# Kernel optimization log

Hardware: AMD Instinct MI355X
Metric: run time of the kernel (lower is better)

Reference implementation:

```python
import jax, jax.numpy as jnp
import numpy as np

DIM = 256
KEY_DIM = 16
NUM_HEADS = 8
ATTN_RATIO = 4
NH_KD = KEY_DIM * NUM_HEADS   # 128
D = ATTN_RATIO * KEY_DIM      # 64
DH = D * NUM_HEADS            # 512
POS_LEN = 16
SCALE = KEY_DIM ** -0.5


def _cbn(x, w, s, b):
    # 1x1 conv (no bias) + folded BatchNorm affine. w: [out,in], x: [B,in,H,W]
    y = jnp.einsum('oi,bihw->bohw', w, x)
    return y * s[None, :, None, None] + b[None, :, None, None]


def _interp_pos(pos, n):
    # F.interpolate(mode='linear', align_corners=False) from length POS_LEN to n.
    L = pos.shape[-1]
    coords = (jnp.arange(n, dtype=pos.dtype) + 0.5) * (L / n) - 0.5
    coords = jnp.clip(coords, 0.0, L - 1)
    lo = jnp.floor(coords).astype(jnp.int32)
    hi = jnp.minimum(lo + 1, L - 1)
    t = coords - lo.astype(pos.dtype)
    return pos[..., lo] * (1 - t) + pos[..., hi] * t  # [1,C,n]


def _axial_attn(q_emb, k_emb, v_emb, pos_q, pos_k, n):
    # q_emb/k_emb: [B,NH_KD,n], v_emb: [B,DH,n]
    B = q_emb.shape[0]
    q = (q_emb + _interp_pos(pos_q, n)).reshape(B, NUM_HEADS, KEY_DIM, n)
    k = (k_emb + _interp_pos(pos_k, n)).reshape(B, NUM_HEADS, KEY_DIM, n)
    v = v_emb.reshape(B, NUM_HEADS, D, n)
    attn = jnp.einsum('bhcn,bhcm->bhnm', q, k) * SCALE
    attn = jax.nn.softmax(attn, axis=-1)
    xx = jnp.einsum('bhnm,bhdm->bhnd', attn, v)      # [B,NH,n,D]
    return xx.transpose(0, 1, 3, 2).reshape(B, DH, n)  # [B,DH,n]


def _forward(x, wq, sq, bq, wk, sk, bk, wv, sv, bv,
             pos_rowq, pos_rowk, pos_colq, pos_colk,
             w_row, s_row, b_row, w_col, s_col, b_col,
             w_proj, s_proj, b_proj, w_sc, s_sc, b_sc,
             w_dw, s_dw, b_dw, w_pw, s_pw, b_pw):
    B, C, H, W = x.shape
    q = _cbn(x, wq, sq, bq)   # [B,NH_KD,H,W]
    k = _cbn(x, wk, sk, bk)
    v = _cbn(x, wv, sv, bv)   # [B,DH,H,W]

    # row branch (mean over W)
    xx_row = _axial_attn(q.mean(-1), k.mean(-1), v.mean(-1), pos_rowq, pos_rowk, H)
    xx_row = _cbn(jax.nn.relu(xx_row[..., None]), w_row, s_row, b_row)      # [B,DH,H,1]
    # column branch (mean over H)
    xx_col = _axial_attn(q.mean(-2), k.mean(-2), v.mean(-2), pos_colq, pos_colk, W)
    xx_col = _cbn(jax.nn.relu(xx_col[:, :, None, :]), w_col, s_col, b_col)  # [B,DH,1,W]

    attn_out = v + (xx_row + xx_col)
    attn_out = _cbn(jax.nn.relu(attn_out), w_proj, s_proj, b_proj)          # [B,DIM,H,W]

    # gate branch: 1x1 -> dw3x3 -> relu -> 1x1 -> h_sigmoid
    gate = _cbn(x, w_sc, s_sc, b_sc)
    gate = jax.lax.conv_general_dilated(
        gate, w_dw, (1, 1), 'SAME',
        dimension_numbers=('NCHW', 'OIHW', 'NCHW'), feature_group_count=DIM)
    gate = gate * s_dw[None, :, None, None] + b_dw[None, :, None, None]
    gate = jax.nn.relu(gate)
    gate = _cbn(gate, w_pw, s_pw, b_pw)
    gate = jnp.clip(gate + 3.0, 0.0, 6.0) / 6.0  # h_sigmoid
    return gate * attn_out


def setup_inputs() -> dict:
    key = jax.random.key(0)
    ks = jax.random.split(key, 32)
    B, H, W = 16, 64, 64
    nrm = lambda k, sh, sc=0.05: jax.random.normal(k, sh, dtype=jnp.float32) * sc
    inp = {
        'x': nrm(ks[0], (B, DIM, H, W), 1.0),
        'wq': nrm(ks[1], (NH_KD, DIM)), 'sq': 1.0 + nrm(ks[2], (NH_KD,)), 'bq': nrm(ks[3], (NH_KD,)),
        'wk': nrm(ks[4], (NH_KD, DIM)), 'sk': 1.0 + nrm(ks[5], (NH_KD,)), 'bk': nrm(ks[6], (NH_KD,)),
        'wv': nrm(ks[7], (DH, DIM)), 'sv': 1.0 + nrm(ks[8], (DH,)), 'bv': nrm(ks[9], (DH,)),
        'pos_rowq': nrm(ks[10], (1, NH_KD, POS_LEN), 1.0), 'pos_rowk': nrm(ks[11], (1, NH_KD, POS_LEN), 1.0),
        'pos_colq': nrm(ks[12], (1, NH_KD, POS_LEN), 1.0), 'pos_colk': nrm(ks[13], (1, NH_KD, POS_LEN), 1.0),
        'w_row': nrm(ks[14], (DH, DH)), 's_row': 1.0 + nrm(ks[15], (DH,)), 'b_row': nrm(ks[16], (DH,)),
        'w_col': nrm(ks[17], (DH, DH)), 's_col': 1.0 + nrm(ks[18], (DH,)), 'b_col': nrm(ks[19], (DH,)),
        'w_proj': nrm(ks[20], (DIM, DH)), 's_proj': 1.0 + nrm(ks[21], (DIM,)), 'b_proj': nrm(ks[22], (DIM,)),
        'w_sc': nrm(ks[23], (DIM, DIM)), 's_sc': 1.0 + nrm(ks[24], (DIM,)), 'b_sc': nrm(ks[25], (DIM,)),
        'w_dw': nrm(ks[26], (DIM, 1, 3, 3)), 's_dw': 1.0 + nrm(ks[27], (DIM,)), 'b_dw': nrm(ks[28], (DIM,)),
        'w_pw': nrm(ks[29], (DIM, DIM)), 's_pw': 1.0 + nrm(ks[30], (DIM,)), 'b_pw': nrm(ks[31], (DIM,)),
    }
    return inp


def reference(x, wq, sq, bq, wk, sk, bk, wv, sv, bv,
              pos_rowq, pos_rowk, pos_colq, pos_colk,
              w_row, s_row, b_row, w_col, s_col, b_col,
              w_proj, s_proj, b_proj, w_sc, s_sc, b_sc,
              w_dw, s_dw, b_dw, w_pw, s_pw, b_pw):
    return _forward(x, wq, sq, bq, wk, sk, bk, wv, sv, bv,
                    pos_rowq, pos_rowk, pos_colq, pos_colk,
                    w_row, s_row, b_row, w_col, s_col, b_col,
                    w_proj, s_proj, b_proj, w_sc, s_sc, b_sc,
                    w_dw, s_dw, b_dw, w_pw, s_pw, b_pw)
```

## Files before the change

kernel.cpp:

```cpp
#include <hip/hip_runtime.h>
#include <math.h>

typedef unsigned short u16;
typedef unsigned int u32;
typedef short short8 __attribute__((ext_vector_type(8)));
typedef float f32x4 __attribute__((ext_vector_type(4)));

#define Bn 16
#define Cc 256
#define Pp 4096
#define DHc 512
#define PTOT 65536
#define SCALE 0.25f

__device__ __forceinline__ float bf2f(u16 u) {
    return __uint_as_float(((u32)u) << 16);
}
__device__ __forceinline__ u16 f2bf(float f) {
    u32 u = __float_as_uint(f);
    u32 lsb = (u >> 16) & 1u;
    u += 0x7fffu + lsb;
    return (u16)(u >> 16);
}

__device__ __forceinline__ void gload16(const u16* g, u16* l) {
    __builtin_amdgcn_global_load_lds(
        (const __attribute__((address_space(1))) void*)(uintptr_t)g,
        (__attribute__((address_space(3))) void*)(u32)(uintptr_t)l,
        16, 0, 0);
}

__global__ __launch_bounds__(256) void mean_kernel(
    const float* __restrict__ x, u16* __restrict__ xmb) {
    __shared__ float plane[64][65];
    int bc = blockIdx.x;
    int b = bc >> 8, c = bc & 255;
    const float* xp = x + (size_t)bc * Pp;
    int tid = threadIdx.x;
#pragma unroll
    for (int k = 0; k < 16; ++k) {
        int idx = tid + k * 256;
        plane[idx >> 6][idx & 63] = xp[idx];
    }
    __syncthreads();
    if (tid < 64) {
        float s = 0.f;
#pragma unroll
        for (int w = 0; w < 64; ++w) s += plane[tid][w];
        xmb[((size_t)b * 64 + tid) * 256 + c] = f2bf(s * (1.f / 64.f));
    } else if (tid < 128) {
        int w = tid - 64;
        float s = 0.f;
#pragma unroll
        for (int h = 0; h < 64; ++h) s += plane[h][w];
        xmb[((size_t)1024 + b * 64 + w) * 256 + c] = f2bf(s * (1.f / 64.f));
    }
}

__global__ __launch_bounds__(256) void xpose_kernel(
    const float* __restrict__ x, u16* __restrict__ xbf) {
    __shared__ float tile[64][65];
    int pb = blockIdx.x;
    int cb = blockIdx.y;
    int b = blockIdx.z;
    int t = threadIdx.x;
    int p_l = t & 63, c_q = t >> 6;
    const float* xp = x + ((size_t)b * Cc + cb * 64) * Pp + pb * 64;
#pragma unroll
    for (int rr = 0; rr < 16; ++rr) {
        int c_l = rr * 4 + c_q;
        tile[p_l][c_l] = xp[(size_t)c_l * Pp + p_l];
    }
    __syncthreads();
    int c_l2 = t & 63, p_q = t >> 6;
    u16* dst = xbf + ((size_t)b * Pp + pb * 64) * Cc + cb * 64;
#pragma unroll
    for (int rr = 0; rr < 16; ++rr) {
        int p_l2 = rr * 4 + p_q;
        dst[(size_t)p_l2 * Cc + c_l2] = f2bf(tile[p_l2][c_l2]);
    }
}

__global__ __launch_bounds__(256) void wconv_kernel(
    const float* __restrict__ wq, const float* __restrict__ wk, const float* __restrict__ wv,
    const float* __restrict__ wsc, const float* __restrict__ wproj, const float* __restrict__ wpw,
    const float* __restrict__ wrow, const float* __restrict__ wcol,
    const float* __restrict__ wdw,
    u16* __restrict__ wqkvb, u16* __restrict__ wscb,
    u16* __restrict__ wprojb, u16* __restrict__ wpwb,
    u16* __restrict__ wrb, u16* __restrict__ wcb, float* __restrict__ wdwT) {
    int t = blockIdx.x * 256 + threadIdx.x;
    if (t < 2304) wdwT[(t % 9) * 256 + (t / 9)] = wdw[t];
    if (t < 32768) wqkvb[t] = f2bf(wq[t]);
    else if (t < 65536) wqkvb[t] = f2bf(wk[t - 32768]);
    else if (t < 196608) wqkvb[t] = f2bf(wv[t - 65536]);
    else if (t < 262144) wscb[t - 196608] = f2bf(wsc[t - 196608]);
    else if (t < 393216) wprojb[t - 262144] = f2bf(wproj[t - 262144]);
    else if (t < 458752) wpwb[t - 393216] = f2bf(wpw[t - 393216]);
    else if (t < 720896) wrb[t - 458752] = f2bf(wrow[t - 458752]);
    else wcb[t - 720896] = f2bf(wcol[t - 720896]);
}

__device__ __forceinline__ void gemm_mainloop(
    const u16* __restrict__ W, const u16* __restrict__ X, int K,
    int o0, size_t prow0, u16* ldsA, u16* ldsB, f32x4 (&acc)[4][4]) {
    int t = threadIdx.x;
    int w = t >> 6, lane = t & 63;
    int sr = (w << 5) + (lane >> 2);
    int ks = (lane & 3) * 8;
    const u16* gA = W + (size_t)(o0 + sr) * K + ks;
    const u16* gB = X + (prow0 + sr) * K + ks;
    u16* lA = ldsA + sr * 32 + ks;
    u16* lB = ldsB + sr * 32 + ks;
    int wo = (w >> 1) * 64, wp = (w & 1) * 64;
    const u16* fA = ldsA + (wo + (lane & 15)) * 32 + ((lane >> 4) * 8);
    const u16* fB = ldsB + (wp + (lane & 15)) * 32 + ((lane >> 4) * 8);

    for (int k0 = 0; k0 < K; k0 += 32) {
        if (k0) __syncthreads();
        gload16(gA + k0, lA);
        gload16(gA + k0 + (size_t)16 * K, lA + 16 * 32);
        gload16(gB + k0, lB);
        gload16(gB + k0 + (size_t)16 * K, lB + 16 * 32);
        __syncthreads();
        short8 a[4], b[4];
#pragma unroll
        for (int i = 0; i < 4; ++i) a[i] = *(const short8*)(fA + i * 16 * 32);
#pragma unroll
        for (int j = 0; j < 4; ++j) b[j] = *(const short8*)(fB + j * 16 * 32);
#pragma unroll
        for (int i = 0; i < 4; ++i)
#pragma unroll
            for (int j = 0; j < 4; ++j)
                acc[i][j] = __builtin_amdgcn_mfma_f32_16x16x32_bf16(a[i], b[j], acc[i][j], 0, 0, 0);
    }
}

__global__ __launch_bounds__(256) void gemm_qkv(
    const u16* __restrict__ Wb, const u16* __restrict__ X,
    const float* __restrict__ sq, const float* __restrict__ bq,
    const float* __restrict__ sk, const float* __restrict__ bk,
    const float* __restrict__ sv, const float* __restrict__ bv,
    const float* __restrict__ posrq, const float* __restrict__ posrk,
    const float* __restrict__ poscq, const float* __restrict__ posck,
    float* __restrict__ qrow, float* __restrict__ krow, float* __restrict__ vrow,
    float* __restrict__ qcol, float* __restrict__ kcol, float* __restrict__ vcol) {
    __shared__ u16 ldsA[128 * 32];
    __shared__ u16 ldsB[128 * 32];
    f32x4 acc[4][4];
#pragma unroll
    for (int i = 0; i < 4; ++i)
#pragma unroll
        for (int j = 0; j < 4; ++j) acc[i][j] = (f32x4){0.f, 0.f, 0.f, 0.f};
    int o0 = blockIdx.x * 128;
    size_t prow0 = (size_t)blockIdx.y * 128;
    gemm_mainloop(Wb, X, 256, o0, prow0, ldsA, ldsB, acc);

    int lane = threadIdx.x & 63, w = threadIdx.x >> 6;
    int wo = (w >> 1) * 64, wp = (w & 1) * 64;
    int quad = lane >> 4, cn = lane & 15;
#pragma unroll
    for (int j = 0; j < 4; ++j) {
        int p = (int)prow0 + wp + j * 16 + cn;
        int branch = p >> 10, loc = p & 1023;
        int b = loc >> 6, n = loc & 63;
        float coords = 0.25f * (float)n - 0.375f;
        coords = fminf(fmaxf(coords, 0.f), 15.f);
        int lo = (int)floorf(coords);
        int hi = min(lo + 1, 15);
        float tt = coords - (float)lo;
#pragma unroll
        for (int i = 0; i < 4; ++i) {
            int o = o0 + wo + i * 16 + quad * 4;
            if (o < 128) {
                const float* pos = branch ? poscq : posrq;
                float* dst = branch ? qcol : qrow;
#pragma unroll
                for (int r = 0; r < 4; ++r) {
                    int c = o + r;
                    float pv = pos[c * 16 + lo] * (1.f - tt) + pos[c * 16 + hi] * tt;
                    dst[b * 8192 + c * 64 + n] = acc[i][j][r] * sq[c] + bq[c] + pv;
                }
            } else if (o < 256) {
                const float* pos = branch ? posck : posrk;
                float* dst = branch ? kcol : krow;
#pragma unroll
                for (int r = 0; r < 4; ++r) {
                    int c = o - 128 + r;
                    float pv = pos[c * 16 + lo] * (1.f - tt) + pos[c * 16 + hi] * tt;
                    dst[b * 8192 + c * 64 + n] = acc[i][j][r] * sk[c] + bk[c] + pv;
                }
            } else {
                float* dst = branch ? vcol : vrow;
#pragma unroll
                for (int r = 0; r < 4; ++r) {
                    int c = o - 256 + r;
                    dst[b * 32768 + c * 64 + n] = acc[i][j][r] * sv[c] + bv[c];
                }
            }
        }
    }
}

__global__ __launch_bounds__(512) void attn_kernel(
    const float* __restrict__ qr, const float* __restrict__ kr, const float* __restrict__ vr,
    const float* __restrict__ qc, const float* __restrict__ kc, const float* __restrict__ vc,
    u16* __restrict__ xxbf) {
    int branch = blockIdx.y;
    const float* q = branch ? qc : qr;
    const float* k = branch ? kc : kr;
    const float* v = branch ? vc : vr;
    int bh = blockIdx.x;
    int b = bh >> 3, h = bh & 7;
    __shared__ float qs[16][64], ks[16][64], vs[64][64];
    int t = threadIdx.x;
#pragma unroll
    for (int i = t; i < 1024; i += 512) {
        int c = i >> 6, nn = i & 63;
        qs[c][nn] = q[b * 8192 + (h * 16 + c) * 64 + nn];
        ks[c][nn] = k[b * 8192 + (h * 16 + c) * 64 + nn];
    }
#pragma unroll
    for (int i = t; i < 4096; i += 512) {
        int d = i >> 6, nn = i & 63;
        vs[d][nn] = v[b * 32768 + (h * 64 + d) * 64 + nn];
    }
    __syncthreads();

    int n = t & 63, dq = t >> 6;
    float qv[16];
#pragma unroll
    for (int c = 0; c < 16; ++c) qv[c] = qs[c][n];

    float s[64];
    float mx = -1e30f;
    for (int m = 0; m < 64; ++m) {
        float acc = 0.f;
#pragma unroll
        for (int c = 0; c < 16; ++c) acc += qv[c] * ks[c][m];
        acc *= SCALE;
        s[m] = acc;
        mx = fmaxf(mx, acc);
    }
    float sum = 0.f;
    for (int m = 0; m < 64; ++m) {
        s[m] = __expf(s[m] - mx);
        sum += s[m];
    }
    float inv = 1.f / sum;
    u16* dst = xxbf + (((size_t)(b * 2 + branch)) * 64 + n) * 512 + h * 64 + dq * 8;
#pragma unroll
    for (int dd = 0; dd < 8; ++dd) {
        int d = dq * 8 + dd;
        float acc = 0.f;
#pragma unroll 8
        for (int m = 0; m < 64; ++m) acc += s[m] * vs[d][m];
        dst[dd] = f2bf(fmaxf(acc * inv, 0.f));
    }
}

__global__ __launch_bounds__(256) void post_gemm(
    const u16* __restrict__ xxbf, const u16* __restrict__ wrb, const u16* __restrict__ wcb,
    const float* __restrict__ s_row, const float* __restrict__ b_row,
    const float* __restrict__ s_col, const float* __restrict__ b_col,
    float* __restrict__ xr2, float* __restrict__ xc2) {
    __shared__ u16 ldsA[64 * 32];
    __shared__ u16 ldsB[256 * 32];
    int o0 = blockIdx.x * 256;
    int b = blockIdx.y;
    int branch = blockIdx.z;
    const u16* A = xxbf + ((size_t)(b * 2 + branch)) * 64 * 512;
    const u16* W = branch ? wcb : wrb;
    const float* ss = branch ? s_col : s_row;
    const float* bb = branch ? b_col : b_row;
    float* dst = (branch ? xc2 : xr2) + (size_t)b * 32768;

    f32x4 acc[4][4];
#pragma unroll
    for (int i = 0; i < 4; ++i)
#pragma unroll
        for (int j = 0; j < 4; ++j) acc[i][j] = (f32x4){0.f, 0.f, 0.f, 0.f};

    int t = threadIdx.x, w = t >> 6, lane = t & 63;
    int ks = (t & 3) * 8;
    const u16* gA = A + (size_t)(t >> 2) * 512 + ks;
    const u16* gB = W + (size_t)(o0 + (t >> 2)) * 512 + ks;
    u16* lA = ldsA + (t >> 2) * 32 + ks;
    u16* lB = ldsB + (t >> 2) * 32 + ks;
    const u16* fA = ldsA + (lane & 15) * 32 + ((lane >> 4) * 8);
    const u16* fB = ldsB + (w * 64 + (lane & 15)) * 32 + ((lane >> 4) * 8);

    for (int k0 = 0; k0 < 512; k0 += 32) {
        if (k0) __syncthreads();
        gload16(gA + k0, lA);
#pragma unroll
        for (int r = 0; r < 4; ++r)
            gload16(gB + k0 + (size_t)r * 64 * 512, lB + r * 64 * 32);
        __syncthreads();
        short8 a[4], bfr[4];
#pragma unroll
        for (int i = 0; i < 4; ++i) a[i] = *(const short8*)(fA + i * 16 * 32);
#pragma unroll
        for (int j = 0; j < 4; ++j) bfr[j] = *(const short8*)(fB + j * 16 * 32);
#pragma unroll
        for (int i = 0; i < 4; ++i)
#pragma unroll
            for (int j = 0; j < 4; ++j)
                acc[i][j] = __builtin_amdgcn_mfma_f32_16x16x32_bf16(a[i], bfr[j], acc[i][j], 0, 0, 0);
    }

    int quad = lane >> 4, cn = lane & 15;
#pragma unroll
    for (int i = 0; i < 4; ++i)
#pragma unroll
        for (int j = 0; j < 4; ++j) {
            int o = o0 + w * 64 + j * 16 + cn;
            float sv_ = ss[o], bv_ = bb[o];
#pragma unroll
            for (int r = 0; r < 4; ++r) {
                int n = i * 16 + quad * 4 + r;
                dst[n * 512 + o] = acc[i][j][r] * sv_ + bv_;
            }
        }
}

__global__ __launch_bounds__(256) void gemm_sc(
    const u16* __restrict__ Wb, const u16* __restrict__ X,
    const float* __restrict__ s, const float* __restrict__ bb, u16* __restrict__ outb) {
    __shared__ u16 ldsA[128 * 32];
    __shared__ u16 ldsB[128 * 32];
    f32x4 acc[4][4];
#pragma unroll
    for (int i = 0; i < 4; ++i)
#pragma unroll
        for (int j = 0; j < 4; ++j) acc[i][j] = (f32x4){0.f, 0.f, 0.f, 0.f};
    int o0 = blockIdx.x * 128;
    size_t prow0 = (size_t)blockIdx.y * 128;
    gemm_mainloop(Wb, X, 256, o0, prow0, ldsA, ldsB, acc);

    int lane = threadIdx.x & 63, w = threadIdx.x >> 6;
    int wo = (w >> 1) * 64, wp = (w & 1) * 64;
    int quad = lane >> 4, cn = lane & 15;
#pragma unroll
    for (int i = 0; i < 4; ++i) {
        int ob = o0 + wo + i * 16 + quad * 4;
        f32x4 s4 = *(const f32x4*)&s[ob];
        f32x4 b4 = *(const f32x4*)&bb[ob];
#pragma unroll
        for (int j = 0; j < 4; ++j) {
            size_t p = prow0 + wp + j * 16 + cn;
            ushort4 o4;
            o4.x = f2bf(acc[i][j][0] * s4[0] + b4[0]);
            o4.y = f2bf(acc[i][j][1] * s4[1] + b4[1]);
            o4.z = f2bf(acc[i][j][2] * s4[2] + b4[2]);
            o4.w = f2bf(acc[i][j][3] * s4[3] + b4[3]);
            *(ushort4*)&outb[p * 256 + ob] = o4;
        }
    }
}

__global__ __launch_bounds__(256) void gemm_pw(
    const u16* __restrict__ Wb, const u16* __restrict__ X,
    const float* __restrict__ s, const float* __restrict__ bb, u16* __restrict__ outb) {
    __shared__ u16 ldsA[128 * 32];
    __shared__ u16 ldsB[128 * 32];
    f32x4 acc[4][4];
#pragma unroll
    for (int i = 0; i < 4; ++i)
#pragma unroll
        for (int j = 0; j < 4; ++j) acc[i][j] = (f32x4){0.f, 0.f, 0.f, 0.f};
    int o0 = blockIdx.x * 128;
    size_t prow0 = (size_t)blockIdx.y * 128;
    gemm_mainloop(Wb, X, 256, o0, prow0, ldsA, ldsB, acc);

    int lane = threadIdx.x & 63, w = threadIdx.x >> 6;
    int wo = (w >> 1) * 64, wp = (w & 1) * 64;
    int quad = lane >> 4, cn = lane & 15;
#pragma unroll
    for (int i = 0; i < 4; ++i) {
        int ob = o0 + wo + i * 16 + quad * 4;
        f32x4 s4 = *(const f32x4*)&s[ob];
        f32x4 b4 = *(const f32x4*)&bb[ob];
#pragma unroll
        for (int j = 0; j < 4; ++j) {
            size_t p = prow0 + wp + j * 16 + cn;
            ushort4 o4;
            o4.x = f2bf(fminf(fmaxf(acc[i][j][0] * s4[0] + b4[0] + 3.f, 0.f), 6.f) * (1.f / 6.f));
            o4.y = f2bf(fminf(fmaxf(acc[i][j][1] * s4[1] + b4[1] + 3.f, 0.f), 6.f) * (1.f / 6.f));
            o4.z = f2bf(fminf(fmaxf(acc[i][j][2] * s4[2] + b4[2] + 3.f, 0.f), 6.f) * (1.f / 6.f));
            o4.w = f2bf(fminf(fmaxf(acc[i][j][3] * s4[3] + b4[3] + 3.f, 0.f), 6.f) * (1.f / 6.f));
            *(ushort4*)&outb[p * 256 + ob] = o4;
        }
    }
}

__global__ __launch_bounds__(512) void fused_vproj(
    const u16* __restrict__ Wv, const u16* __restrict__ Wp,
    const u16* __restrict__ X,
    const float* __restrict__ sv, const float* __restrict__ bv,
    const float* __restrict__ xr2, const float* __restrict__ xc2,
    const float* __restrict__ sp, const float* __restrict__ bp,
    const u16* __restrict__ gate, float* __restrict__ out) {
    __shared__ u16 abt[64 * 512];
    __shared__ u16 ldsA[512 * 32];
    __shared__ u16 ldsB[64 * 32];

    int t = threadIdx.x;
    int lane = t & 63, w = t >> 6;
    int quad = lane >> 4, cn = lane & 15;
    int p0 = blockIdx.x * 64;
    int bi = p0 >> 12;
    int hh = (p0 >> 6) & 63;

    f32x4 acc1[4][4];
#pragma unroll
    for (int i = 0; i < 4; ++i)
#pragma unroll
        for (int j = 0; j < 4; ++j) acc1[i][j] = (f32x4){0.f, 0.f, 0.f, 0.f};

    int rowA = t >> 2, seg = t & 3;
    int ow = w * 64;
    const u16* fA = ldsA + (ow + cn) * 32 + quad * 8;
    const u16* fB = ldsB + cn * 32 + quad * 8;

    for (int k0 = 0; k0 < 256; k0 += 32) {
        if (k0) __syncthreads();
#pragma unroll
        for (int kk = 0; kk < 4; ++kk)
            gload16(Wv + (size_t)(rowA + kk * 128) * 256 + k0 + seg * 8,
                    ldsA + ((size_t)t + kk * 512) * 8);
        if (t < 256)
            gload16(X + ((size_t)p0 + rowA) * 256 + k0 + seg * 8, ldsB + (size_t)t * 8);
        __syncthreads();
        short8 a[4], b[4];
#pragma unroll
        for (int i = 0; i < 4; ++i) a[i] = *(const short8*)(fA + i * 16 * 32);
#pragma unroll
        for (int j = 0; j < 4; ++j) b[j] = *(const short8*)(fB + j * 16 * 32);
#pragma unroll
        for (int i = 0; i < 4; ++i)
#pragma unroll
            for (int j = 0; j < 4; ++j)
                acc1[i][j] = __builtin_amdgcn_mfma_f32_16x16x32_bf16(a[i], b[j], acc1[i][j], 0, 0, 0);
    }

#pragma unroll
    for (int i = 0; i < 4; ++i) {
        int ob = ow + i * 16 + quad * 4;
        f32x4 s4 = *(const f32x4*)&sv[ob];
        f32x4 b4 = *(const f32x4*)&bv[ob];
        f32x4 ra = *(const f32x4*)&xr2[(size_t)bi * 32768 + hh * 512 + ob];
#pragma unroll
        for (int j = 0; j < 4; ++j) {
            int p = j * 16 + cn;
            f32x4 ca = *(const f32x4*)&xc2[(size_t)bi * 32768 + p * 512 + ob];
            ushort4 o4;
            o4.x = f2bf(fmaxf(acc1[i][j][0] * s4[0] + b4[0] + ra[0] + ca[0], 0.f));
            o4.y = f2bf(fmaxf(acc1[i][j][1] * s4[1] + b4[1] + ra[1] + ca[1], 0.f));
            o4.z = f2bf(fmaxf(acc1[i][j][2] * s4[2] + b4[2] + ra[2] + ca[2], 0.f));
            o4.w = f2bf(fmaxf(acc1[i][j][3] * s4[3] + b4[3] + ra[3] + ca[3], 0.f));
            *(ushort4*)&abt[p * 512 + (ob ^ ((p & 7) << 3))] = o4;
        }
    }
    __syncthreads();

    f32x4 acc2[4][2];
#pragma unroll
    for (int i = 0; i < 4; ++i)
#pragma unroll
        for (int j = 0; j < 2; ++j) acc2[i][j] = (f32x4){0.f, 0.f, 0.f, 0.f};

    int o2w = (w & 3) * 64, pw = (w >> 2) * 32;
    const u16* fA2 = ldsA + (o2w + cn) * 32 + quad * 8;
    int kfrag = quad * 8;

    for (int k0 = 0; k0 < 512; k0 += 32) {
        if (k0) __syncthreads();
        gload16(Wp + (size_t)rowA * 512 + k0 + seg * 8, ldsA + (size_t)t * 8);
        gload16(Wp + ((size_t)rowA + 128) * 512 + k0 + seg * 8, ldsA + ((size_t)t + 512) * 8);
        __syncthreads();
        short8 a2[4], b2[2];
#pragma unroll
        for (int i = 0; i < 4; ++i) a2[i] = *(const short8*)(fA2 + i * 16 * 32);
#pragma unroll
        for (int j = 0; j < 2; ++j) {
            int p = pw + j * 16 + cn;
            int kk = k0 + kfrag;
            b2[j] = *(const short8*)&abt[p * 512 + (kk ^ ((p & 7) << 3))];
        }
#pragma unroll
        for (int i = 0; i < 4; ++i)
#pragma unroll
            for (int j = 0; j < 2; ++j)
                acc2[i][j] = __builtin_amdgcn_mfma_f32_16x16x32_bf16(a2[i], b2[j], acc2[i][j], 0, 0, 0);
    }

    int pl = p0 & 4095;
#pragma unroll
    for (int i = 0; i < 4; ++i) {
        int ob = o2w + i * 16 + quad * 4;
        f32x4 s4 = *(const f32x4*)&sp[ob];
        f32x4 b4 = *(const f32x4*)&bp[ob];
#pragma unroll
        for (int j = 0; j < 2; ++j) {
            int p = pw + j * 16 + cn;
            size_t pg = (size_t)p0 + p;
            ushort4 gv = *(const ushort4*)&gate[pg * 256 + ob];
            float* op = out + (size_t)bi * 1048576 + (size_t)ob * 4096 + (pl + p);
            op[0 * 4096] = bf2f(gv.x) * (acc2[i][j][0] * s4[0] + b4[0]);
            op[1 * 4096] = bf2f(gv.y) * (acc2[i][j][1] * s4[1] + b4[1]);
            op[2 * 4096] = bf2f(gv.z) * (acc2[i][j][2] * s4[2] + b4[2]);
            op[3 * 4096] = bf2f(gv.w) * (acc2[i][j][3] * s4[3] + b4[3]);
        }
    }
}

__global__ __launch_bounds__(256) void dw_kernel(
    const u16* __restrict__ sc, const float* __restrict__ wdwT,
    const float* __restrict__ sdw, const float* __restrict__ bdw, u16* __restrict__ dwout) {
    int t = blockIdx.x * 256 + threadIdx.x;
    int cg = (t & 31) * 8;
    size_t p = (size_t)(t >> 5);
    int h = (int)((p >> 6) & 63), w_ = (int)(p & 63);
    float acc[8] = {0.f, 0.f, 0.f, 0.f, 0.f, 0.f, 0.f, 0.f};
#pragma unroll
    for (int ky = 0; ky < 3; ++ky) {
        int hh = h + ky - 1;
        if (hh < 0 || hh > 63) continue;
#pragma unroll
        for (int kx = 0; kx < 3; ++kx) {
            int wx = w_ + kx - 1;
            if (wx < 0 || wx > 63) continue;
            size_t pp = (size_t)((long long)p + (ky - 1) * 64 + (kx - 1));
            short8 v = *(const short8*)&sc[pp * 256 + cg];
            const float* wt = &wdwT[(ky * 3 + kx) * 256 + cg];
            f32x4 w0 = *(const f32x4*)wt;
            f32x4 w1 = *(const f32x4*)(wt + 4);
            acc[0] += w0[0] * bf2f((u16)v[0]); acc[1] += w0[1] * bf2f((u16)v[1]);
            acc[2] += w0[2] * bf2f((u16)v[2]); acc[3] += w0[3] * bf2f((u16)v[3]);
            acc[4] += w1[0] * bf2f((u16)v[4]); acc[5] += w1[1] * bf2f((u16)v[5]);
            acc[6] += w1[2] * bf2f((u16)v[6]); acc[7] += w1[3] * bf2f((u16)v[7]);
        }
    }
    f32x4 s0 = *(const f32x4*)&sdw[cg], s1 = *(const f32x4*)&sdw[cg + 4];
    f32x4 b0 = *(const f32x4*)&bdw[cg], b1 = *(const f32x4*)&bdw[cg + 4];
    short8 o;
    o[0] = (short)f2bf(fmaxf(acc[0] * s0[0] + b0[0], 0.f));
    o[1] = (short)f2bf(fmaxf(acc[1] * s0[1] + b0[1], 0.f));
    o[2] = (short)f2bf(fmaxf(acc[2] * s0[2] + b0[2], 0.f));
    o[3] = (short)f2bf(fmaxf(acc[3] * s0[3] + b0[3], 0.f));
    o[4] = (short)f2bf(fmaxf(acc[4] * s1[0] + b1[0], 0.f));
    o[5] = (short)f2bf(fmaxf(acc[5] * s1[1] + b1[1], 0.f));
    o[6] = (short)f2bf(fmaxf(acc[6] * s1[2] + b1[2], 0.f));
    o[7] = (short)f2bf(fmaxf(acc[7] * s1[3] + b1[3], 0.f));
    *(short8*)&dwout[p * 256 + cg] = o;
}

extern "C" void kernel_launch(void* const* d_in, const int* in_sizes, int n_in,
                              void* d_out, int out_size, void* d_ws, size_t ws_size,
                              hipStream_t stream) {
    const float* x = (const float*)d_in[0];
    const float* wq = (const float*)d_in[1];
    const float* sq = (const float*)d_in[2];
    const float* bq = (const float*)d_in[3];
    const float* wk = (const float*)d_in[4];
    const float* sk = (const float*)d_in[5];
    const float* bk = (const float*)d_in[6];
    const float* wv = (const float*)d_in[7];
    const float* sv = (const float*)d_in[8];
    const float* bv = (const float*)d_in[9];
    const float* posrq = (const float*)d_in[10];
    const float* posrk = (const float*)d_in[11];
    const float* poscq = (const float*)d_in[12];
    const float* posck = (const float*)d_in[13];
    const float* w_row = (const float*)d_in[14];
    const float* s_row = (const float*)d_in[15];
    const float* b_row = (const float*)d_in[16];
    const float* w_col = (const float*)d_in[17];
    const float* s_col = (const float*)d_in[18];
    const float* b_col = (const float*)d_in[19];
    const float* w_proj = (const float*)d_in[20];
    const float* s_proj = (const float*)d_in[21];
    const float* b_proj = (const float*)d_in[22];
    const float* w_sc = (const float*)d_in[23];
    const float* s_sc = (const float*)d_in[24];
    const float* b_sc = (const float*)d_in[25];
    const float* w_dw = (const float*)d_in[26];
    const float* s_dw = (const float*)d_in[27];
    const float* b_dw = (const float*)d_in[28];
    const float* w_pw = (const float*)d_in[29];
    const float* s_pw = (const float*)d_in[30];
    const float* b_pw = (const float*)d_in[31];
    float* out = (float*)d_out;

    float* fws = (float*)d_ws;
    float* qrow = fws;
    float* krow = qrow + 131072;
    float* qcol = krow + 131072;
    float* kcol = qcol + 131072;
    float* vrow = kcol + 131072;
    float* vcol = vrow + 524288;
    float* xr2  = vcol + 524288;
    float* xc2  = xr2 + 524288;
    float* wdwT = xc2 + 524288;
    u16* xmb    = (u16*)(wdwT + 2304);
    u16* xbf    = xmb + 524288;
    u16* wqkvb  = xbf + (size_t)PTOT * 256;
    u16* wscb   = wqkvb + 196608;
    u16* wprojb = wscb + 65536;
    u16* wpwb   = wprojb + 131072;
    u16* wrb    = wpwb + 65536;
    u16* wcb    = wrb + 262144;
    u16* xxbf   = wcb + 262144;
    u16* scb    = xxbf + 1048576;
    u16* dwb    = scb + (size_t)PTOT * 256;
    u16* gate   = scb;

    mean_kernel<<<dim3(Bn * Cc), 256, 0, stream>>>(x, xmb);
    xpose_kernel<<<dim3(64, 4, Bn), 256, 0, stream>>>(x, xbf);
    wconv_kernel<<<dim3(3840), 256, 0, stream>>>(
        wq, wk, wv, w_sc, w_proj, w_pw, w_row, w_col, w_dw,
        wqkvb, wscb, wprojb, wpwb, wrb, wcb, wdwT);
    gemm_qkv<<<dim3(6, 16), 256, 0, stream>>>(
        wqkvb, xmb, sq, bq, sk, bk, sv, bv,
        posrq, posrk, poscq, posck, qrow, krow, vrow, qcol, kcol, vcol);
    attn_kernel<<<dim3(128, 2), 512, 0, stream>>>(qrow, krow, vrow, qcol, kcol, vcol, xxbf);
    post_gemm<<<dim3(2, Bn, 2), 256, 0, stream>>>(
        xxbf, wrb, wcb, s_row, b_row, s_col, b_col, xr2, xc2);
    gemm_sc<<<dim3(2, 512), 256, 0, stream>>>(wscb, xbf, s_sc, b_sc, scb);
    dw_kernel<<<dim3(8192), 256, 0, stream>>>(scb, wdwT, s_dw, b_dw, dwb);
    gemm_pw<<<dim3(2, 512), 256, 0, stream>>>(wpwb, dwb, s_pw, b_pw, gate);
    fused_vproj<<<dim3(1024), 512, 0, stream>>>(
        wqkvb + 65536, wprojb, xbf, sv, bv, xr2, xc2, s_proj, b_proj, gate, out);
}
```

Baseline: 459.0 us.

## Load weights directly from global into registers and share one LDS buffer

The fused V-projection kernel no longer stages Wv and Wp tiles through LDS with per-k-step barriers. Each wave now reads its weight fragments straight from global memory (cache-resident). The full 64-pixel X tile is preloaded once into a swizzled LDS buffer, and that buffer is reused for the intermediate activation tile. The second GEMM is remapped so each wave owns 32 output channels across all 64 pixels, and launch bounds request 4 blocks per CU. This removes most barriers and cuts LDS footprint to raise occupancy, but it relies on L1/L2 for weight reuse across waves and blocks.

```diff
diff --git a/kernel.cpp b/kernel.cpp
--- a/kernel.cpp
+++ b/kernel.cpp
@@ -394,55 +394,64 @@
     }
 }
 
-__global__ __launch_bounds__(512) void fused_vproj(
+__global__ __launch_bounds__(512, 4) void fused_vproj(
     const u16* __restrict__ Wv, const u16* __restrict__ Wp,
     const u16* __restrict__ X,
     const float* __restrict__ sv, const float* __restrict__ bv,
     const float* __restrict__ xr2, const float* __restrict__ xc2,
     const float* __restrict__ sp, const float* __restrict__ bp,
     const u16* __restrict__ gate, float* __restrict__ out) {
-    __shared__ u16 abt[64 * 512];
-    __shared__ u16 ldsA[512 * 32];
-    __shared__ u16 ldsB[64 * 32];
+    __shared__ u16 lds[64 * 512];
 
     int t = threadIdx.x;
     int lane = t & 63, w = t >> 6;
     int quad = lane >> 4, cn = lane & 15;
+    int ppx = cn & 7;
     int p0 = blockIdx.x * 64;
     int bi = p0 >> 12;
     int hh = (p0 >> 6) & 63;
 
+#pragma unroll
+    for (int r = 0; r < 4; ++r) {
+        int li = r * 512 + t;
+        int p = li >> 5, ko = li & 31;
+        gload16(X + ((size_t)(p0 + p)) * 256 + ((ko ^ (p & 7)) << 3),
+                lds + (size_t)li * 8);
+    }
+    __syncthreads();
+
     f32x4 acc1[4][4];
 #pragma unroll
     for (int i = 0; i < 4; ++i)
 #pragma unroll
         for (int j = 0; j < 4; ++j) acc1[i][j] = (f32x4){0.f, 0.f, 0.f, 0.f};
 
-    int rowA = t >> 2, seg = t & 3;
     int ow = w * 64;
-    const u16* fA = ldsA + (ow + cn) * 32 + quad * 8;
-    const u16* fB = ldsB + cn * 32 + quad * 8;
+    const u16* gA0 = Wv + (size_t)(ow + cn) * 256 + quad * 8;
+    const u16* gA1 = gA0 + (size_t)16 * 256;
+    const u16* gA2 = gA0 + (size_t)32 * 256;
+    const u16* gA3 = gA0 + (size_t)48 * 256;
 
     for (int k0 = 0; k0 < 256; k0 += 32) {
-        if (k0) __syncthreads();
-#pragma unroll
-        for (int kk = 0; kk < 4; ++kk)
-            gload16(Wv + (size_t)(rowA + kk * 128) * 256 + k0 + seg * 8,
-                    ldsA + ((size_t)t + kk * 512) * 8);
-        if (t < 256)
-            gload16(X + ((size_t)p0 + rowA) * 256 + k0 + seg * 8, ldsB + (size_t)t * 8);
-        __syncthreads();
+        int og = (k0 >> 3) + quad;
         short8 a[4], b[4];
-#pragma unroll
-        for (int i = 0; i < 4; ++i) a[i] = *(const short8*)(fA + i * 16 * 32);
-#pragma unroll
-        for (int j = 0; j < 4; ++j) b[j] = *(const short8*)(fB + j * 16 * 32);
+        a[0] = *(const short8*)(gA0 + k0);
+        a[1] = *(const short8*)(gA1 + k0);
+        a[2] = *(const short8*)(gA2 + k0);
+        a[3] = *(const short8*)(gA3 + k0);
+#pragma unroll
+        for (int j = 0; j < 4; ++j) {
+            int pl = j * 16 + cn;
+            b[j] = *(const short8*)&lds[pl * 256 + ((og ^ ppx) << 3)];
+        }
 #pragma unroll
         for (int i = 0; i < 4; ++i)
 #pragma unroll
             for (int j = 0; j < 4; ++j)
                 acc1[i][j] = __builtin_amdgcn_mfma_f32_16x16x32_bf16(a[i], b[j], acc1[i][j], 0, 0, 0);
     }
+
+    __syncthreads();
 
 #pragma unroll
     for (int i = 0; i < 4; ++i) {
@@ -459,54 +468,50 @@
             o4.y = f2bf(fmaxf(acc1[i][j][1] * s4[1] + b4[1] + ra[1] + ca[1], 0.f));
             o4.z = f2bf(fmaxf(acc1[i][j][2] * s4[2] + b4[2] + ra[2] + ca[2], 0.f));
             o4.w = f2bf(fmaxf(acc1[i][j][3] * s4[3] + b4[3] + ra[3] + ca[3], 0.f));
-            *(ushort4*)&abt[p * 512 + (ob ^ ((p & 7) << 3))] = o4;
+            *(ushort4*)&lds[p * 512 + (ob ^ ((p & 7) << 3))] = o4;
         }
     }
     __syncthreads();
 
-    f32x4 acc2[4][2];
-#pragma unroll
-    for (int i = 0; i < 4; ++i)
-#pragma unroll
-        for (int j = 0; j < 2; ++j) acc2[i][j] = (f32x4){0.f, 0.f, 0.f, 0.f};
-
-    int o2w = (w & 3) * 64, pw = (w >> 2) * 32;
-    const u16* fA2 = ldsA + (o2w + cn) * 32 + quad * 8;
-    int kfrag = quad * 8;
+    f32x4 acc2[2][4];
+#pragma unroll
+    for (int i = 0; i < 2; ++i)
+#pragma unroll
+        for (int j = 0; j < 4; ++j) acc2[i][j] = (f32x4){0.f, 0.f, 0.f, 0.f};
+
+    int o2w = w * 32;
+    const u16* gP0 = Wp + (size_t)(o2w + cn) * 512 + quad * 8;
+    const u16* gP1 = gP0 + (size_t)16 * 512;
 
     for (int k0 = 0; k0 < 512; k0 += 32) {
-        if (k0) __syncthreads();
-        gload16(Wp + (size_t)rowA * 512 + k0 + seg * 8, ldsA + (size_t)t * 8);
-        gload16(Wp + ((size_t)rowA + 128) * 512 + k0 + seg * 8, ldsA + ((size_t)t + 512) * 8);
-        __syncthreads();
-        short8 a2[4], b2[2];
-#pragma unroll
-        for (int i = 0; i < 4; ++i) a2[i] = *(const short8*)(fA2 + i * 16 * 32);
-#pragma unroll
-        for (int j = 0; j < 2; ++j) {
-            int p = pw + j * 16 + cn;
-            int kk = k0 + kfrag;
-            b2[j] = *(const short8*)&abt[p * 512 + (kk ^ ((p & 7) << 3))];
-        }
-#pragma unroll
-        for (int i = 0; i < 4; ++i)
-#pragma unroll
-            for (int j = 0; j < 2; ++j)
+        short8 a2[2], b2[4];
+        a2[0] = *(const short8*)(gP0 + k0);
+        a2[1] = *(const short8*)(gP1 + k0);
+        int kk = k0 + quad * 8;
+#pragma unroll
+        for (int j = 0; j < 4; ++j) {
+            int p = j * 16 + cn;
+            b2[j] = *(const short8*)&lds[p * 512 + (kk ^ ((p & 7) << 3))];
+        }
+#pragma unroll
+        for (int i = 0; i < 2; ++i)
+#pragma unroll
+            for (int j = 0; j < 4; ++j)
                 acc2[i][j] = __builtin_amdgcn_mfma_f32_16x16x32_bf16(a2[i], b2[j], acc2[i][j], 0, 0, 0);
     }
 
-    int pl = p0 & 4095;
-#pragma unroll
-    for (int i = 0; i < 4; ++i) {
+    int pl0 = p0 & 4095;
+#pragma unroll
+    for (int i = 0; i < 2; ++i) {
         int ob = o2w + i * 16 + quad * 4;
         f32x4 s4 = *(const f32x4*)&sp[ob];
         f32x4 b4 = *(const f32x4*)&bp[ob];
 #pragma unroll
-        for (int j = 0; j < 2; ++j) {
-            int p = pw + j * 16 + cn;
+        for (int j = 0; j < 4; ++j) {
+            int p = j * 16 + cn;
             size_t pg = (size_t)p0 + p;
             ushort4 gv = *(const ushort4*)&gate[pg * 256 + ob];
-            float* op = out + (size_t)bi * 1048576 + (size_t)ob * 4096 + (pl + p);
+            float* op = out + (size_t)bi * 1048576 + (size_t)ob * 4096 + (pl0 + p);
             op[0 * 4096] = bf2f(gv.x) * (acc2[i][j][0] * s4[0] + b4[0]);
             op[1 * 4096] = bf2f(gv.y) * (acc2[i][j][1] * s4[1] + b4[1]);
             op[2 * 4096] = bf2f(gv.z) * (acc2[i][j][2] * s4[2] + b4[2]);
```

Measured after the change: 460.6 us. No clear change (+0.4%).
